# Optimization experiments

Measured on AMD Instinct MI355X. Metric: run time of the kernel, lower is better.

## Reference

```python
import jax, jax.numpy as jnp
import numpy as np

B, N, C, H = 2, 2048, 768, 12
HD = C // H
SCALE = HD ** -0.5


def setup_inputs() -> dict:
    key = jax.random.key(0)
    k1, k2, k3, k4 = jax.random.split(key, 4)
    return {
        "x": jax.random.normal(k1, (B, N, C), dtype=jnp.float32),
        "qkv_w": jax.random.normal(k2, (3 * C, C), dtype=jnp.float32) * (C ** -0.5),
        "proj_w": jax.random.normal(k3, (C, C), dtype=jnp.float32) * (C ** -0.5),
        "proj_b": jax.random.normal(k4, (C,), dtype=jnp.float32) * 0.01,
    }


def reference(x, qkv_w, proj_w, proj_b):
    b, n, c = x.shape
    # qkv: Linear(dim, 3*dim, bias=False) -> (B,N,3,H,HD) -> per-tensor (B,H,N,HD)
    qkv = (x @ qkv_w.T).reshape(b, n, 3, H, HD)
    q, k, v = jnp.moveaxis(qkv, 2, 0)          # each (B,N,H,HD)
    q = q.transpose(0, 2, 1, 3)                # (B,H,N,HD)
    k = k.transpose(0, 2, 1, 3)
    v = v.transpose(0, 2, 1, 3)
    attn_logits = jnp.einsum("bhqd,bhkd->bhqk", q, k) * SCALE  # (B,H,N,N)
    attn = jax.nn.softmax(attn_logits, axis=-1)
    score = jnp.mean(attn, axis=1)             # (B,N,N) mean over heads
    # dropout p=0.0 -> identity
    out = jnp.einsum("bhqk,bhkd->bhqd", attn, v)  # (B,H,N,HD)
    out = out.transpose(0, 2, 1, 3).reshape(b, n, c)
    out = out @ proj_w.T + proj_b
    return out, score
```

## Files before the change

kernel.cpp:

```cpp
#include <hip/hip_runtime.h>
#include <cstddef>

typedef __attribute__((ext_vector_type(8))) short bf16x8;
typedef __attribute__((ext_vector_type(4))) float f32x4;

constexpr int Bb = 2, Nn = 2048, Cc = 768, Hh = 12, HDd = 64;
constexpr float QSCALE = 0.125f * 1.44269504088896340736f;

__device__ inline short f2bf(float f) {
  unsigned u = __builtin_bit_cast(unsigned, f);
  u += 0x7fff + ((u >> 16) & 1);
  return (short)(u >> 16);
}
__device__ inline unsigned cvtpk(float a, float b) {
  unsigned r;
  asm("v_cvt_pk_bf16_f32 %0, %1, %2" : "=v"(r) : "v"(a), "v"(b));
  return r;
}
__device__ inline void gl_lds16(const void* g, void* l) {
  __builtin_amdgcn_global_load_lds(
      (const __attribute__((address_space(1))) unsigned*)g,
      (__attribute__((address_space(3))) unsigned*)l, 16, 0, 0);
}
__device__ inline bf16x8 lds8(const short* p) { return *(const bf16x8*)p; }
__device__ inline bf16x8 ld_frag(const short* base, int row, int ch) {
  return *(const bf16x8*)&base[row * 64 + (((ch ^ (row & 7)) << 3))];
}

__global__ __launch_bounds__(256) void cvt_kernel(const float* __restrict__ s,
                                                  short* __restrict__ d) {
  const int i = (blockIdx.x * 256 + threadIdx.x) * 4;
  const float4 v = *(const float4*)&s[i];
  short4 o;
  o.x = f2bf(v.x); o.y = f2bf(v.y); o.z = f2bf(v.z); o.w = f2bf(v.w);
  *(short4*)&d[i] = o;
}

__global__ __launch_bounds__(256) void qkv_mfma(
    const short* __restrict__ A, const short* __restrict__ W,
    short* __restrict__ Qg, short* __restrict__ Kg, short* __restrict__ Vtg) {
  __shared__ short As[128 * 64];
  __shared__ short Bs[128 * 64];
  const int t = threadIdx.x, l = t & 63, w = t >> 6;
  const int lr = l & 15, lh = l >> 4;
  const int m0 = blockIdx.x * 128, r0 = blockIdx.y * 128;
  const int wr = w >> 1, wc = w & 1;
  f32x4 acc[4][4];
#pragma unroll
  for (int i = 0; i < 4; ++i)
#pragma unroll
    for (int j = 0; j < 4; ++j) acc[i][j] = (f32x4){0.f, 0.f, 0.f, 0.f};

  for (int k0 = 0; k0 < Cc; k0 += 64) {
    __syncthreads();
#pragma unroll
    for (int u = 0; u < 4; ++u) {
      const int du = (w * 4 + u) * 64 + l;
      const int row = du >> 3, ch = du & 7, sch = ch ^ (row & 7);
      gl_lds16(A + (size_t)(m0 + row) * Cc + k0 + sch * 8,
               &As[(w * 4 + u) * 512]);
      gl_lds16(W + (size_t)(r0 + row) * Cc + k0 + sch * 8,
               &Bs[(w * 4 + u) * 512]);
    }
    __syncthreads();
#pragma unroll
    for (int kp = 0; kp < 2; ++kp) {
      bf16x8 af[4], bfv[4];
#pragma unroll
      for (int i = 0; i < 4; ++i)
        af[i] = ld_frag(As, wr * 64 + i * 16 + lr, kp * 4 + lh);
#pragma unroll
      for (int j = 0; j < 4; ++j)
        bfv[j] = ld_frag(Bs, wc * 64 + j * 16 + lr, kp * 4 + lh);
#pragma unroll
      for (int i = 0; i < 4; ++i)
#pragma unroll
        for (int j = 0; j < 4; ++j)
          acc[i][j] = __builtin_amdgcn_mfma_f32_16x16x32_bf16(
              af[i], bfv[j], acc[i][j], 0, 0, 0);
    }
  }
  const int which = r0 / Cc;
  const int rbase = r0 % Cc;
  const int bq = m0 >> 11;
  const int nb = (m0 & 2047) + wr * 64;
  if (which == 2) {
#pragma unroll
    for (int j = 0; j < 4; ++j) {
      const int rr = rbase + wc * 64 + j * 16 + lr;
      const int head = rr >> 6, dd = rr & 63;
      short* vp = &Vtg[(((size_t)bq * Hh + head) * HDd + dd) * Nn];
#pragma unroll
      for (int i = 0; i < 4; ++i) {
        short4 o;
        o.x = f2bf(acc[i][j][0]); o.y = f2bf(acc[i][j][1]);
        o.z = f2bf(acc[i][j][2]); o.w = f2bf(acc[i][j][3]);
        *(short4*)&vp[nb + i * 16 + lh * 4] = o;
      }
    }
  } else {
    const float scl = (which == 0) ? QSCALE : 1.0f;
    short* __restrict__ dst = (which == 0) ? Qg : Kg;
#pragma unroll
    for (int j = 0; j < 4; ++j) {
      const int rr = rbase + wc * 64 + j * 16 + lr;
      const int head = rr >> 6, dd = rr & 63;
      short* dp = &dst[((size_t)bq * Hh + head) * Nn * HDd + dd];
#pragma unroll
      for (int i = 0; i < 4; ++i)
#pragma unroll
        for (int r = 0; r < 4; ++r)
          dp[(size_t)(nb + i * 16 + lh * 4 + r) * HDd] =
              f2bf(acc[i][j][r] * scl);
    }
  }
}

__global__ __launch_bounds__(256, 3) void attn_pass1(
    const short* __restrict__ Qg, const short* __restrict__ Kg,
    const short* __restrict__ Vtg, float* __restrict__ Linv,
    short* __restrict__ OHb) {
  __shared__ short SM[2 * 8192 + 4 * 1024];
  __shared__ float LinvS[64];
  const int t = threadIdx.x, l = t & 63, w = t >> 6;
  const int lr = l & 15, lh = l >> 4;
  const int bid0 = blockIdx.x;
  const int bid = (bid0 & 7) * 96 + (bid0 >> 3);
  const int q0 = (bid & 31) * 64;
  const int head = (bid >> 5) % Hh;
  const int b = bid / (32 * Hh);
  const size_t base = (size_t)b * Hh + head;
  const short* Qh = Qg + base * Nn * HDd;
  const short* Kh = Kg + base * Nn * HDd;
  const short* Vh = Vtg + base * HDd * Nn;
  const int qw = q0 + w * 16;
  const int PB = 16384 + w * 1024;

  int fof[2][4], pof[2], wof[4];
#pragma unroll
  for (int kp = 0; kp < 2; ++kp) {
#pragma unroll
    for (int i = 0; i < 4; ++i)
      fof[kp][i] = (i * 16 + lr) * 64 + (((kp * 4 + lh) ^ (lr & 7)) << 3);
    pof[kp] = lr * 64 + (((kp * 4 + lh) ^ (lr & 7)) << 3);
  }
#pragma unroll
  for (int i = 0; i < 4; ++i) {
    const int ch = 2 * i + (lh >> 1);
    wof[i] = lr * 64 + ((ch ^ (lr & 7)) << 3) + (lh & 1) * 4;
  }

  bf16x8 qf[2];
#pragma unroll
  for (int kp = 0; kp < 2; ++kp)
    qf[kp] = *(const bf16x8*)&Qh[(size_t)(qw + lr) * HDd + kp * 32 + lh * 8];

  f32x4 accO[4];
#pragma unroll
  for (int j = 0; j < 4; ++j) accO[j] = (f32x4){0.f, 0.f, 0.f, 0.f};
  float Lp = 0.f;

  auto stage = [&](const int buf, const int tile) {
    const short* Kt = Kh + (size_t)tile * (64 * HDd);
    const short* Vt = Vh + tile * 64;
#pragma unroll
    for (int u = 0; u < 2; ++u) {
      const int du = (w * 2 + u) * 64 + l;
      const int row = du >> 3, ch = du & 7, sch = ch ^ (row & 7);
      gl_lds16(Kt + row * 64 + sch * 8, &SM[buf * 8192 + (w * 2 + u) * 512]);
      gl_lds16(Vt + (size_t)row * Nn + sch * 8,
               &SM[buf * 8192 + 4096 + (w * 2 + u) * 512]);
    }
  };

  auto compute = [&](const int kb) {
    f32x4 sacc[4];
#pragma unroll
    for (int i = 0; i < 4; ++i) sacc[i] = (f32x4){0.f, 0.f, 0.f, 0.f};
    __builtin_amdgcn_s_setprio(1);
#pragma unroll
    for (int kp = 0; kp < 2; ++kp)
#pragma unroll
      for (int i = 0; i < 4; ++i)
        sacc[i] = __builtin_amdgcn_mfma_f32_16x16x32_bf16(
            lds8(&SM[kb + fof[kp][i]]), qf[kp], sacc[i], 0, 0, 0);
    __builtin_amdgcn_s_setprio(0);
#pragma unroll
    for (int i = 0; i < 4; ++i) {
      const float p0 = exp2f(sacc[i][0]), p1 = exp2f(sacc[i][1]);
      const float p2 = exp2f(sacc[i][2]), p3 = exp2f(sacc[i][3]);
      Lp += (p0 + p1) + (p2 + p3);
      uint2 pk;
      pk.x = cvtpk(p0, p1);
      pk.y = cvtpk(p2, p3);
      *(uint2*)&SM[PB + wof[i]] = pk;
    }
    __builtin_amdgcn_s_setprio(1);
#pragma unroll
    for (int kp = 0; kp < 2; ++kp) {
      const bf16x8 pa = lds8(&SM[PB + pof[kp]]);
#pragma unroll
      for (int j = 0; j < 4; ++j)
        accO[j] = __builtin_amdgcn_mfma_f32_16x16x32_bf16(
            pa, lds8(&SM[kb + 4096 + fof[kp][j]]), accO[j], 0, 0, 0);
    }
    __builtin_amdgcn_s_setprio(0);
  };

  stage(0, 0);
  __syncthreads();
#pragma unroll 1
  for (int it = 0; it < Nn / 64; it += 2) {
    stage(1, it + 1);
    compute(0);
    __syncthreads();
    if (it + 2 < Nn / 64) stage(0, it + 2);
    compute(8192);
    __syncthreads();
  }

  Lp += __shfl_xor(Lp, 16, 64);
  Lp += __shfl_xor(Lp, 32, 64);
  const float linv = 1.0f / Lp;
  if (lh == 0) {
    Linv[base * Nn + qw + lr] = linv;
    LinvS[w * 16 + lr] = linv;
  }
  __syncthreads();
#pragma unroll
  for (int j = 0; j < 4; ++j) {
#pragma unroll
    for (int r = 0; r < 4; ++r) {
      const int ql = lh * 4 + r;
      const float li = LinvS[w * 16 + ql];
      OHb[((size_t)b * Nn + qw + ql) * Cc + head * HDd + j * 16 + lr] =
          f2bf(accO[j][r] * li);
    }
  }
}

__global__ __launch_bounds__(256, 4) void score_mfma(
    const short* __restrict__ Qg, const short* __restrict__ Kg,
    const float* __restrict__ Linv, float* __restrict__ score) {
  __shared__ short SM[2 * 8192];
  const int t = threadIdx.x, l = t & 63, w = t >> 6;
  const int lr = l & 15, lh = l >> 4;
  const int kv0 = blockIdx.x * 64, q0 = blockIdx.y * 64, b = blockIdx.z;
  const int qw = q0 + w * 16;

  int fof[2][4];
#pragma unroll
  for (int kp = 0; kp < 2; ++kp)
#pragma unroll
    for (int i = 0; i < 4; ++i)
      fof[kp][i] = (i * 16 + lr) * 64 + (((kp * 4 + lh) ^ (lr & 7)) << 3);

  f32x4 sc[4];
#pragma unroll
  for (int i = 0; i < 4; ++i) sc[i] = (f32x4){0.f, 0.f, 0.f, 0.f};

  auto stage = [&](const int buf, const int h) {
    const short* Kt = Kg + (((size_t)b * Hh + h) * Nn + kv0) * HDd;
    const short* Qt = Qg + (((size_t)b * Hh + h) * Nn + q0) * HDd;
#pragma unroll
    for (int u = 0; u < 2; ++u) {
      const int du = (w * 2 + u) * 64 + l;
      const int row = du >> 3, ch = du & 7, sch = ch ^ (row & 7);
      gl_lds16(Kt + row * 64 + sch * 8, &SM[buf * 8192 + (w * 2 + u) * 512]);
      gl_lds16(Qt + row * 64 + sch * 8,
               &SM[buf * 8192 + 4096 + (w * 2 + u) * 512]);
    }
  };

  auto compute = [&](const int kb, const int h) {
    const float linv = Linv[((size_t)b * Hh + h) * Nn + qw + lr];
    const bf16x8 q0f = lds8(&SM[kb + 4096 + fof[0][w]]);
    const bf16x8 q1f = lds8(&SM[kb + 4096 + fof[1][w]]);
    f32x4 sacc[4];
#pragma unroll
    for (int i = 0; i < 4; ++i) sacc[i] = (f32x4){0.f, 0.f, 0.f, 0.f};
    __builtin_amdgcn_s_setprio(1);
#pragma unroll
    for (int i = 0; i < 4; ++i)
      sacc[i] = __builtin_amdgcn_mfma_f32_16x16x32_bf16(
          lds8(&SM[kb + fof[0][i]]), q0f, sacc[i], 0, 0, 0);
#pragma unroll
    for (int i = 0; i < 4; ++i)
      sacc[i] = __builtin_amdgcn_mfma_f32_16x16x32_bf16(
          lds8(&SM[kb + fof[1][i]]), q1f, sacc[i], 0, 0, 0);
    __builtin_amdgcn_s_setprio(0);
#pragma unroll
    for (int i = 0; i < 4; ++i)
#pragma unroll
      for (int r = 0; r < 4; ++r) sc[i][r] += exp2f(sacc[i][r]) * linv;
  };

  stage(0, 0);
  __syncthreads();
#pragma unroll 1
  for (int h = 0; h < Hh; h += 2) {
    stage(1, h + 1);
    compute(0, h);
    __syncthreads();
    if (h + 2 < Hh) stage(0, h + 2);
    compute(8192, h + 1);
    __syncthreads();
  }

  constexpr float invH = 1.0f / 12.0f;
#pragma unroll
  for (int i = 0; i < 4; ++i) {
    f32x4 o;
#pragma unroll
    for (int r = 0; r < 4; ++r) o[r] = sc[i][r] * invH;
    *(f32x4*)&score[((size_t)b * Nn + qw + lr) * Nn + kv0 + i * 16 + lh * 4] =
        o;
  }
}

__global__ __launch_bounds__(256) void proj_mfma(
    const short* __restrict__ A, const short* __restrict__ W,
    const float* __restrict__ bias, float* __restrict__ out) {
  __shared__ short As[128 * 64];
  __shared__ short Bs[128 * 64];
  const int t = threadIdx.x, l = t & 63, w = t >> 6;
  const int lr = l & 15, lh = l >> 4;
  const int m0 = blockIdx.x * 128, c0 = blockIdx.y * 128;
  const int wr = w >> 1, wc = w & 1;
  f32x4 acc[4][4];
#pragma unroll
  for (int i = 0; i < 4; ++i)
#pragma unroll
    for (int j = 0; j < 4; ++j) acc[i][j] = (f32x4){0.f, 0.f, 0.f, 0.f};

  for (int k0 = 0; k0 < Cc; k0 += 64) {
    __syncthreads();
#pragma unroll
    for (int u = 0; u < 4; ++u) {
      const int du = (w * 4 + u) * 64 + l;
      const int row = du >> 3, ch = du & 7, sch = ch ^ (row & 7);
      gl_lds16(A + (size_t)(m0 + row) * Cc + k0 + sch * 8,
               &As[(w * 4 + u) * 512]);
      gl_lds16(W + (size_t)(c0 + row) * Cc + k0 + sch * 8,
               &Bs[(w * 4 + u) * 512]);
    }
    __syncthreads();
#pragma unroll
    for (int kp = 0; kp < 2; ++kp) {
      bf16x8 af[4], bfv[4];
#pragma unroll
      for (int i = 0; i < 4; ++i)
        af[i] = ld_frag(As, wr * 64 + i * 16 + lr, kp * 4 + lh);
#pragma unroll
      for (int j = 0; j < 4; ++j)
        bfv[j] = ld_frag(Bs, wc * 64 + j * 16 + lr, kp * 4 + lh);
#pragma unroll
      for (int i = 0; i < 4; ++i)
#pragma unroll
        for (int j = 0; j < 4; ++j)
          acc[i][j] = __builtin_amdgcn_mfma_f32_16x16x32_bf16(
              af[i], bfv[j], acc[i][j], 0, 0, 0);
    }
  }
#pragma unroll
  for (int j = 0; j < 4; ++j) {
    const int c = c0 + wc * 64 + j * 16 + lr;
    const float bi = bias[c];
#pragma unroll
    for (int i = 0; i < 4; ++i)
#pragma unroll
      for (int r = 0; r < 4; ++r) {
        const int m = m0 + wr * 64 + i * 16 + lh * 4 + r;
        out[(size_t)m * Cc + c] = acc[i][j][r] + bi;
      }
  }
}

extern "C" void kernel_launch(void* const* d_in, const int* in_sizes, int n_in,
                              void* d_out, int out_size, void* d_ws,
                              size_t ws_size, hipStream_t stream) {
  const float* x = (const float*)d_in[0];
  const float* qkv_w = (const float*)d_in[1];
  const float* proj_w = (const float*)d_in[2];
  const float* proj_b = (const float*)d_in[3];

  float* out = (float*)d_out;
  float* score = out + (size_t)Bb * Nn * Cc;

  const size_t nx = (size_t)Bb * Nn * Cc;
  const size_t nwq = (size_t)3 * Cc * Cc;
  const size_t npw = (size_t)Cc * Cc;
  short* xb = (short*)d_ws;
  short* wqb = xb + nx;
  short* pwb = wqb + nwq;
  short* Qb = pwb + npw;
  short* Kb = Qb + nx;
  short* Vtb = Kb + nx;
  short* OHb = Vtb + nx;
  float* Linv = (float*)(OHb + nx);

  cvt_kernel<<<dim3((int)(nx / 1024)), 256, 0, stream>>>(x, xb);
  cvt_kernel<<<dim3((int)(nwq / 1024)), 256, 0, stream>>>(qkv_w, wqb);
  cvt_kernel<<<dim3((int)(npw / 1024)), 256, 0, stream>>>(proj_w, pwb);
  qkv_mfma<<<dim3(32, 18), 256, 0, stream>>>(xb, wqb, Qb, Kb, Vtb);
  attn_pass1<<<dim3(Bb * Hh * 32), 256, 0, stream>>>(Qb, Kb, Vtb, Linv, OHb);
  score_mfma<<<dim3(32, 32, Bb), 256, 0, stream>>>(Qb, Kb, Linv, score);
  proj_mfma<<<dim3(32, 6), 256, 0, stream>>>(OHb, pwb, proj_b, out);
}
```

Measured before the change: 144.2 us.

## Switch attention and score kernels to 32x32x16 MFMA with register-resident P

Rewrites the attention pass to use 32x32x16 bf16 MFMA with two 64-thread waves each handling 32 query rows. The P matrix is repacked in registers with v_permlane32_swap instead of round-tripping through LDS. The score kernel also moves to 32x32 MFMA over 128-query tiles, loading Q fragments directly from global memory and staging only K in LDS. It also remaps block indices per XCD for locality. The goal is fewer LDS writes and barriers and fewer MFMA issues, at the cost of changed occupancy and more registers per thread.

```diff
diff --git a/kernel.cpp b/kernel.cpp
--- a/kernel.cpp
+++ b/kernel.cpp
@@ -3,6 +3,8 @@
 
 typedef __attribute__((ext_vector_type(8))) short bf16x8;
 typedef __attribute__((ext_vector_type(4))) float f32x4;
+typedef __attribute__((ext_vector_type(16))) float f32x16;
+typedef __attribute__((ext_vector_type(4))) unsigned u32x4;
 
 constexpr int Bb = 2, Nn = 2048, Cc = 768, Hh = 12, HDd = 64;
 constexpr float QSCALE = 0.125f * 1.44269504088896340736f;
@@ -17,12 +19,25 @@
   asm("v_cvt_pk_bf16_f32 %0, %1, %2" : "=v"(r) : "v"(a), "v"(b));
   return r;
 }
+__device__ inline void pl32swap(unsigned& a, unsigned& b) {
+  asm("v_permlane32_swap_b32 %0, %1" : "+v"(a), "+v"(b));
+}
 __device__ inline void gl_lds16(const void* g, void* l) {
   __builtin_amdgcn_global_load_lds(
       (const __attribute__((address_space(1))) unsigned*)g,
       (__attribute__((address_space(3))) unsigned*)l, 16, 0, 0);
 }
 __device__ inline bf16x8 lds8(const short* p) { return *(const bf16x8*)p; }
+__device__ inline bf16x8 mk8(unsigned a, unsigned b, unsigned c, unsigned d) {
+  u32x4 t = {a, b, c, d};
+  return __builtin_bit_cast(bf16x8, t);
+}
+__device__ inline f32x16 zero16() {
+  f32x16 z;
+#pragma unroll
+  for (int r = 0; r < 16; ++r) z[r] = 0.f;
+  return z;
+}
 __device__ inline bf16x8 ld_frag(const short* base, int row, int ch) {
   return *(const bf16x8*)&base[row * 64 + (((ch ^ (row & 7)) << 3))];
 }
@@ -116,16 +131,15 @@
   }
 }
 
-__global__ __launch_bounds__(256, 3) void attn_pass1(
+__global__ __launch_bounds__(128) void attn_pass1(
     const short* __restrict__ Qg, const short* __restrict__ Kg,
     const short* __restrict__ Vtg, float* __restrict__ Linv,
     short* __restrict__ OHb) {
-  __shared__ short SM[2 * 8192 + 4 * 1024];
-  __shared__ float LinvS[64];
+  __shared__ short SM[4 * 4096];
   const int t = threadIdx.x, l = t & 63, w = t >> 6;
-  const int lr = l & 15, lh = l >> 4;
-  const int bid0 = blockIdx.x;
-  const int bid = (bid0 & 7) * 96 + (bid0 >> 3);
+  const int lo5 = l & 31, hi5 = l >> 5;
+  const int raw = blockIdx.x;
+  const int bid = (raw & 7) * 96 + (raw >> 3);
   const int q0 = (bid & 31) * 64;
   const int head = (bid >> 5) % Hh;
   const int b = bid / (32 * Hh);
@@ -133,188 +147,223 @@
   const short* Qh = Qg + base * Nn * HDd;
   const short* Kh = Kg + base * Nn * HDd;
   const short* Vh = Vtg + base * HDd * Nn;
-  const int qw = q0 + w * 16;
-  const int PB = 16384 + w * 1024;
-
-  int fof[2][4], pof[2], wof[4];
-#pragma unroll
-  for (int kp = 0; kp < 2; ++kp) {
-#pragma unroll
-    for (int i = 0; i < 4; ++i)
-      fof[kp][i] = (i * 16 + lr) * 64 + (((kp * 4 + lh) ^ (lr & 7)) << 3);
-    pof[kp] = lr * 64 + (((kp * 4 + lh) ^ (lr & 7)) << 3);
-  }
-#pragma unroll
-  for (int i = 0; i < 4; ++i) {
-    const int ch = 2 * i + (lh >> 1);
-    wof[i] = lr * 64 + ((ch ^ (lr & 7)) << 3) + (lh & 1) * 4;
-  }
-
-  bf16x8 qf[2];
-#pragma unroll
-  for (int kp = 0; kp < 2; ++kp)
-    qf[kp] = *(const bf16x8*)&Qh[(size_t)(qw + lr) * HDd + kp * 32 + lh * 8];
-
-  f32x4 accO[4];
-#pragma unroll
-  for (int j = 0; j < 4; ++j) accO[j] = (f32x4){0.f, 0.f, 0.f, 0.f};
+  const int qw = q0 + w * 32;
+
+  int of2[2][4];
+#pragma unroll
+  for (int i = 0; i < 2; ++i)
+#pragma unroll
+    for (int s = 0; s < 4; ++s)
+      of2[i][s] = (i * 32 + lo5) * 64 + ((((2 * s + hi5) ^ (l & 7))) << 3);
+
+  bf16x8 qf[4];
+#pragma unroll
+  for (int s = 0; s < 4; ++s)
+    qf[s] = *(const bf16x8*)&Qh[(size_t)(qw + lo5) * HDd + s * 16 + hi5 * 8];
+
+  f32x16 accO0 = zero16(), accO1 = zero16();
   float Lp = 0.f;
 
   auto stage = [&](const int buf, const int tile) {
     const short* Kt = Kh + (size_t)tile * (64 * HDd);
     const short* Vt = Vh + tile * 64;
 #pragma unroll
-    for (int u = 0; u < 2; ++u) {
-      const int du = (w * 2 + u) * 64 + l;
+    for (int u = 0; u < 4; ++u) {
+      const int cu = u * 2 + w;
+      const int du = cu * 64 + l;
       const int row = du >> 3, ch = du & 7, sch = ch ^ (row & 7);
-      gl_lds16(Kt + row * 64 + sch * 8, &SM[buf * 8192 + (w * 2 + u) * 512]);
+      gl_lds16(Kt + row * 64 + sch * 8, &SM[buf * 4096 + cu * 512]);
       gl_lds16(Vt + (size_t)row * Nn + sch * 8,
-               &SM[buf * 8192 + 4096 + (w * 2 + u) * 512]);
+               &SM[8192 + buf * 4096 + cu * 512]);
     }
   };
 
   auto compute = [&](const int kb) {
-    f32x4 sacc[4];
-#pragma unroll
-    for (int i = 0; i < 4; ++i) sacc[i] = (f32x4){0.f, 0.f, 0.f, 0.f};
-    __builtin_amdgcn_s_setprio(1);
-#pragma unroll
-    for (int kp = 0; kp < 2; ++kp)
-#pragma unroll
-      for (int i = 0; i < 4; ++i)
-        sacc[i] = __builtin_amdgcn_mfma_f32_16x16x32_bf16(
-            lds8(&SM[kb + fof[kp][i]]), qf[kp], sacc[i], 0, 0, 0);
-    __builtin_amdgcn_s_setprio(0);
-#pragma unroll
-    for (int i = 0; i < 4; ++i) {
-      const float p0 = exp2f(sacc[i][0]), p1 = exp2f(sacc[i][1]);
-      const float p2 = exp2f(sacc[i][2]), p3 = exp2f(sacc[i][3]);
-      Lp += (p0 + p1) + (p2 + p3);
-      uint2 pk;
-      pk.x = cvtpk(p0, p1);
-      pk.y = cvtpk(p2, p3);
-      *(uint2*)&SM[PB + wof[i]] = pk;
-    }
-    __builtin_amdgcn_s_setprio(1);
-#pragma unroll
-    for (int kp = 0; kp < 2; ++kp) {
-      const bf16x8 pa = lds8(&SM[PB + pof[kp]]);
-#pragma unroll
-      for (int j = 0; j < 4; ++j)
-        accO[j] = __builtin_amdgcn_mfma_f32_16x16x32_bf16(
-            pa, lds8(&SM[kb + 4096 + fof[kp][j]]), accO[j], 0, 0, 0);
-    }
-    __builtin_amdgcn_s_setprio(0);
+    const int vb = 8192 + kb;
+    f32x16 s0 = zero16(), s1 = zero16();
+#pragma unroll
+    for (int s = 0; s < 4; ++s)
+      s0 = __builtin_amdgcn_mfma_f32_32x32x16_bf16(lds8(&SM[kb + of2[0][s]]),
+                                                   qf[s], s0, 0, 0, 0);
+#pragma unroll
+    for (int s = 0; s < 4; ++s)
+      s1 = __builtin_amdgcn_mfma_f32_32x32x16_bf16(lds8(&SM[kb + of2[1][s]]),
+                                                   qf[s], s1, 0, 0, 0);
+    float p[16];
+#pragma unroll
+    for (int r = 0; r < 16; ++r) { p[r] = exp2f(s0[r]); Lp += p[r]; }
+    unsigned a0 = cvtpk(p[0], p[1]), b0 = cvtpk(p[2], p[3]);
+    unsigned c0 = cvtpk(p[4], p[5]), d0 = cvtpk(p[6], p[7]);
+    pl32swap(a0, c0); pl32swap(b0, d0);
+    const bf16x8 pa0 = mk8(a0, b0, c0, d0);
+    unsigned a1 = cvtpk(p[8], p[9]), b1 = cvtpk(p[10], p[11]);
+    unsigned c1 = cvtpk(p[12], p[13]), d1 = cvtpk(p[14], p[15]);
+    pl32swap(a1, c1); pl32swap(b1, d1);
+    const bf16x8 pa1 = mk8(a1, b1, c1, d1);
+#pragma unroll
+    for (int r = 0; r < 16; ++r) { p[r] = exp2f(s1[r]); Lp += p[r]; }
+    unsigned a2 = cvtpk(p[0], p[1]), b2 = cvtpk(p[2], p[3]);
+    unsigned c2 = cvtpk(p[4], p[5]), d2 = cvtpk(p[6], p[7]);
+    pl32swap(a2, c2); pl32swap(b2, d2);
+    const bf16x8 pa2 = mk8(a2, b2, c2, d2);
+    unsigned a3 = cvtpk(p[8], p[9]), b3 = cvtpk(p[10], p[11]);
+    unsigned c3 = cvtpk(p[12], p[13]), d3 = cvtpk(p[14], p[15]);
+    pl32swap(a3, c3); pl32swap(b3, d3);
+    const bf16x8 pa3 = mk8(a3, b3, c3, d3);
+    accO0 = __builtin_amdgcn_mfma_f32_32x32x16_bf16(lds8(&SM[vb + of2[0][0]]),
+                                                    pa0, accO0, 0, 0, 0);
+    accO1 = __builtin_amdgcn_mfma_f32_32x32x16_bf16(lds8(&SM[vb + of2[1][0]]),
+                                                    pa0, accO1, 0, 0, 0);
+    accO0 = __builtin_amdgcn_mfma_f32_32x32x16_bf16(lds8(&SM[vb + of2[0][1]]),
+                                                    pa1, accO0, 0, 0, 0);
+    accO1 = __builtin_amdgcn_mfma_f32_32x32x16_bf16(lds8(&SM[vb + of2[1][1]]),
+                                                    pa1, accO1, 0, 0, 0);
+    accO0 = __builtin_amdgcn_mfma_f32_32x32x16_bf16(lds8(&SM[vb + of2[0][2]]),
+                                                    pa2, accO0, 0, 0, 0);
+    accO1 = __builtin_amdgcn_mfma_f32_32x32x16_bf16(lds8(&SM[vb + of2[1][2]]),
+                                                    pa2, accO1, 0, 0, 0);
+    accO0 = __builtin_amdgcn_mfma_f32_32x32x16_bf16(lds8(&SM[vb + of2[0][3]]),
+                                                    pa3, accO0, 0, 0, 0);
+    accO1 = __builtin_amdgcn_mfma_f32_32x32x16_bf16(lds8(&SM[vb + of2[1][3]]),
+                                                    pa3, accO1, 0, 0, 0);
   };
 
   stage(0, 0);
   __syncthreads();
 #pragma unroll 1
-  for (int it = 0; it < Nn / 64; it += 2) {
+  for (int it = 0; it < 32; it += 2) {
     stage(1, it + 1);
     compute(0);
     __syncthreads();
-    if (it + 2 < Nn / 64) stage(0, it + 2);
-    compute(8192);
-    __syncthreads();
-  }
-
-  Lp += __shfl_xor(Lp, 16, 64);
-  Lp += __shfl_xor(Lp, 32, 64);
+    if (it + 2 < 32) stage(0, it + 2);
+    compute(4096);
+    __syncthreads();
+  }
+
+  Lp += __shfl_xor(Lp, 32);
   const float linv = 1.0f / Lp;
-  if (lh == 0) {
-    Linv[base * Nn + qw + lr] = linv;
-    LinvS[w * 16 + lr] = linv;
-  }
-  __syncthreads();
-#pragma unroll
-  for (int j = 0; j < 4; ++j) {
-#pragma unroll
-    for (int r = 0; r < 4; ++r) {
-      const int ql = lh * 4 + r;
-      const float li = LinvS[w * 16 + ql];
-      OHb[((size_t)b * Nn + qw + ql) * Cc + head * HDd + j * 16 + lr] =
-          f2bf(accO[j][r] * li);
-    }
-  }
-}
-
-__global__ __launch_bounds__(256, 4) void score_mfma(
+  const int qv = qw + lo5;
+  if (hi5 == 0) Linv[base * Nn + qv] = linv;
+#pragma unroll
+  for (int dh = 0; dh < 2; ++dh) {
+#pragma unroll
+    for (int g = 0; g < 4; ++g) {
+      short4 o;
+      if (dh == 0) {
+        o.x = f2bf(accO0[4 * g + 0] * linv); o.y = f2bf(accO0[4 * g + 1] * linv);
+        o.z = f2bf(accO0[4 * g + 2] * linv); o.w = f2bf(accO0[4 * g + 3] * linv);
+      } else {
+        o.x = f2bf(accO1[4 * g + 0] * linv); o.y = f2bf(accO1[4 * g + 1] * linv);
+        o.z = f2bf(accO1[4 * g + 2] * linv); o.w = f2bf(accO1[4 * g + 3] * linv);
+      }
+      *(short4*)&OHb[((size_t)b * Nn + qv) * Cc + head * HDd + dh * 32 +
+                     8 * g + 4 * hi5] = o;
+    }
+  }
+}
+
+__global__ __launch_bounds__(256, 3) void score_mfma(
     const short* __restrict__ Qg, const short* __restrict__ Kg,
     const float* __restrict__ Linv, float* __restrict__ score) {
-  __shared__ short SM[2 * 8192];
+  __shared__ short SK[2 * 4096];
   const int t = threadIdx.x, l = t & 63, w = t >> 6;
-  const int lr = l & 15, lh = l >> 4;
-  const int kv0 = blockIdx.x * 64, q0 = blockIdx.y * 64, b = blockIdx.z;
-  const int qw = q0 + w * 16;
-
-  int fof[2][4];
-#pragma unroll
-  for (int kp = 0; kp < 2; ++kp)
-#pragma unroll
-    for (int i = 0; i < 4; ++i)
-      fof[kp][i] = (i * 16 + lr) * 64 + (((kp * 4 + lh) ^ (lr & 7)) << 3);
-
-  f32x4 sc[4];
-#pragma unroll
-  for (int i = 0; i < 4; ++i) sc[i] = (f32x4){0.f, 0.f, 0.f, 0.f};
-
-  auto stage = [&](const int buf, const int h) {
+  const int lo5 = l & 31, hi5 = l >> 5;
+  const int raw = blockIdx.x;
+  const int xcd = raw & 7, idx = raw >> 3;
+  const int b = xcd >> 2;
+  const int q0 = ((xcd & 3) * 4 + (idx >> 5)) * 128;
+  const int kv0 = (idx & 31) * 64;
+  const int qw = q0 + w * 32;
+
+  int of2[2][4];
+#pragma unroll
+  for (int i = 0; i < 2; ++i)
+#pragma unroll
+    for (int s = 0; s < 4; ++s)
+      of2[i][s] = (i * 32 + lo5) * 64 + ((((2 * s + hi5) ^ (l & 7))) << 3);
+
+  f32x16 sc0 = zero16(), sc1 = zero16();
+
+  auto stage = [&](const int kb, const int h) {
     const short* Kt = Kg + (((size_t)b * Hh + h) * Nn + kv0) * HDd;
-    const short* Qt = Qg + (((size_t)b * Hh + h) * Nn + q0) * HDd;
 #pragma unroll
     for (int u = 0; u < 2; ++u) {
-      const int du = (w * 2 + u) * 64 + l;
+      const int cu = u * 4 + w;
+      const int du = cu * 64 + l;
       const int row = du >> 3, ch = du & 7, sch = ch ^ (row & 7);
-      gl_lds16(Kt + row * 64 + sch * 8, &SM[buf * 8192 + (w * 2 + u) * 512]);
-      gl_lds16(Qt + row * 64 + sch * 8,
-               &SM[buf * 8192 + 4096 + (w * 2 + u) * 512]);
+      gl_lds16(Kt + row * 64 + sch * 8, &SK[kb + cu * 512]);
     }
   };
-
-  auto compute = [&](const int kb, const int h) {
-    const float linv = Linv[((size_t)b * Hh + h) * Nn + qw + lr];
-    const bf16x8 q0f = lds8(&SM[kb + 4096 + fof[0][w]]);
-    const bf16x8 q1f = lds8(&SM[kb + 4096 + fof[1][w]]);
-    f32x4 sacc[4];
-#pragma unroll
-    for (int i = 0; i < 4; ++i) sacc[i] = (f32x4){0.f, 0.f, 0.f, 0.f};
-    __builtin_amdgcn_s_setprio(1);
-#pragma unroll
-    for (int i = 0; i < 4; ++i)
-      sacc[i] = __builtin_amdgcn_mfma_f32_16x16x32_bf16(
-          lds8(&SM[kb + fof[0][i]]), q0f, sacc[i], 0, 0, 0);
-#pragma unroll
-    for (int i = 0; i < 4; ++i)
-      sacc[i] = __builtin_amdgcn_mfma_f32_16x16x32_bf16(
-          lds8(&SM[kb + fof[1][i]]), q1f, sacc[i], 0, 0, 0);
-    __builtin_amdgcn_s_setprio(0);
-#pragma unroll
-    for (int i = 0; i < 4; ++i)
-#pragma unroll
-      for (int r = 0; r < 4; ++r) sc[i][r] += exp2f(sacc[i][r]) * linv;
+  auto ldq = [&](const int h, bf16x8& f0, bf16x8& f1, bf16x8& f2, bf16x8& f3) {
+    const short* Qh = Qg + ((size_t)b * Hh + h) * Nn * HDd;
+    f0 = *(const bf16x8*)&Qh[(size_t)(qw + lo5) * HDd + 0 * 16 + hi5 * 8];
+    f1 = *(const bf16x8*)&Qh[(size_t)(qw + lo5) * HDd + 1 * 16 + hi5 * 8];
+    f2 = *(const bf16x8*)&Qh[(size_t)(qw + lo5) * HDd + 2 * 16 + hi5 * 8];
+    f3 = *(const bf16x8*)&Qh[(size_t)(qw + lo5) * HDd + 3 * 16 + hi5 * 8];
   };
-
+  auto head_step = [&](const int kb, const bf16x8 f0, const bf16x8 f1,
+                       const bf16x8 f2, const bf16x8 f3, const float lv) {
+    f32x16 s0 = zero16(), s1 = zero16();
+    s0 = __builtin_amdgcn_mfma_f32_32x32x16_bf16(lds8(&SK[kb + of2[0][0]]), f0,
+                                                 s0, 0, 0, 0);
+    s1 = __builtin_amdgcn_mfma_f32_32x32x16_bf16(lds8(&SK[kb + of2[1][0]]), f0,
+                                                 s1, 0, 0, 0);
+    s0 = __builtin_amdgcn_mfma_f32_32x32x16_bf16(lds8(&SK[kb + of2[0][1]]), f1,
+                                                 s0, 0, 0, 0);
+    s1 = __builtin_amdgcn_mfma_f32_32x32x16_bf16(lds8(&SK[kb + of2[1][1]]), f1,
+                                                 s1, 0, 0, 0);
+    s0 = __builtin_amdgcn_mfma_f32_32x32x16_bf16(lds8(&SK[kb + of2[0][2]]), f2,
+                                                 s0, 0, 0, 0);
+    s1 = __builtin_amdgcn_mfma_f32_32x32x16_bf16(lds8(&SK[kb + of2[1][2]]), f2,
+                                                 s1, 0, 0, 0);
+    s0 = __builtin_amdgcn_mfma_f32_32x32x16_bf16(lds8(&SK[kb + of2[0][3]]), f3,
+                                                 s0, 0, 0, 0);
+    s1 = __builtin_amdgcn_mfma_f32_32x32x16_bf16(lds8(&SK[kb + of2[1][3]]), f3,
+                                                 s1, 0, 0, 0);
+#pragma unroll
+    for (int r = 0; r < 16; ++r) {
+      sc0[r] += exp2f(s0[r]) * lv;
+      sc1[r] += exp2f(s1[r]) * lv;
+    }
+  };
+
+  bf16x8 qA0, qA1, qA2, qA3, qB0, qB1, qB2, qB3;
   stage(0, 0);
+  ldq(0, qA0, qA1, qA2, qA3);
   __syncthreads();
 #pragma unroll 1
   for (int h = 0; h < Hh; h += 2) {
-    stage(1, h + 1);
-    compute(0, h);
-    __syncthreads();
-    if (h + 2 < Hh) stage(0, h + 2);
-    compute(8192, h + 1);
+    stage(4096, h + 1);
+    ldq(h + 1, qB0, qB1, qB2, qB3);
+    {
+      const float lv = Linv[((size_t)b * Hh + h) * Nn + qw + lo5];
+      head_step(0, qA0, qA1, qA2, qA3, lv);
+    }
+    __syncthreads();
+    if (h + 2 < Hh) {
+      stage(0, h + 2);
+      ldq(h + 2, qA0, qA1, qA2, qA3);
+    }
+    {
+      const float lv = Linv[((size_t)b * Hh + h + 1) * Nn + qw + lo5];
+      head_step(4096, qB0, qB1, qB2, qB3, lv);
+    }
     __syncthreads();
   }
 
   constexpr float invH = 1.0f / 12.0f;
-#pragma unroll
-  for (int i = 0; i < 4; ++i) {
-    f32x4 o;
-#pragma unroll
-    for (int r = 0; r < 4; ++r) o[r] = sc[i][r] * invH;
-    *(f32x4*)&score[((size_t)b * Nn + qw + lr) * Nn + kv0 + i * 16 + lh * 4] =
-        o;
+  const int qv = qw + lo5;
+#pragma unroll
+  for (int g = 0; g < 4; ++g) {
+    f32x4 o0, o1;
+#pragma unroll
+    for (int e = 0; e < 4; ++e) {
+      o0[e] = sc0[4 * g + e] * invH;
+      o1[e] = sc1[4 * g + e] * invH;
+    }
+    *(f32x4*)&score[((size_t)b * Nn + qv) * Nn + kv0 + 8 * g + 4 * hi5] = o0;
+    *(f32x4*)&score[((size_t)b * Nn + qv) * Nn + kv0 + 32 + 8 * g + 4 * hi5] =
+        o1;
   }
 }
 
@@ -403,7 +452,7 @@
   cvt_kernel<<<dim3((int)(nwq / 1024)), 256, 0, stream>>>(qkv_w, wqb);
   cvt_kernel<<<dim3((int)(npw / 1024)), 256, 0, stream>>>(proj_w, pwb);
   qkv_mfma<<<dim3(32, 18), 256, 0, stream>>>(xb, wqb, Qb, Kb, Vtb);
-  attn_pass1<<<dim3(Bb * Hh * 32), 256, 0, stream>>>(Qb, Kb, Vtb, Linv, OHb);
-  score_mfma<<<dim3(32, 32, Bb), 256, 0, stream>>>(Qb, Kb, Linv, score);
+  attn_pass1<<<dim3(768), 128, 0, stream>>>(Qb, Kb, Vtb, Linv, OHb);
+  score_mfma<<<dim3(1024), 256, 0, stream>>>(Qb, Kb, Linv, score);
   proj_mfma<<<dim3(32, 6), 256, 0, stream>>>(OHb, pwb, proj_b, out);
 }
```

Measured after the change: 160.1 us. 11.0% more time.
